# Kernel optimization log

Hardware: AMD Instinct MI355X
Metric: run time of the kernel (lower is better)

Reference implementation:

```python
import jax, jax.numpy as jnp
import numpy as np
from jax import lax

K = 7          # kernel_size
GROUPS = 16    # channels // group_channels
GC = 16        # group_channels
C = 256        # channels
PAD = (K - 1) // 2
BN_EPS = 1e-5


def setup_inputs() -> dict:
    key = jax.random.key(0)
    ks = jax.random.split(key, 8)
    B, H, W = 4, 56, 56
    x = jax.random.normal(ks[0], (B, C, H, W), jnp.float32)
    y = jax.random.normal(ks[1], (B, C, H, W), jnp.float32)
    # conv1: 1x1 conv (bias=False since followed by BN), C -> C//4
    w1 = jax.random.normal(ks[2], (C // 4, C), jnp.float32) * (1.0 / np.sqrt(C))
    gamma = jnp.ones((C // 4,), jnp.float32)
    beta = jnp.zeros((C // 4,), jnp.float32)
    mean = jax.random.normal(ks[3], (C // 4,), jnp.float32) * 0.1
    var = jax.random.uniform(ks[4], (C // 4,), jnp.float32, 0.5, 1.5)
    # conv2: 1x1 conv with bias, C//4 -> k^2 * groups
    w2 = jax.random.normal(ks[5], (K * K * GROUPS, C // 4), jnp.float32) * (1.0 / np.sqrt(C // 4))
    b2 = jnp.zeros((K * K * GROUPS,), jnp.float32)
    return {"x": x, "y": y, "w1": w1, "gamma": gamma, "beta": beta,
            "mean": mean, "var": var, "w2": w2, "b2": b2}


def reference(x, y, w1, gamma, beta, mean, var, w2, b2):
    # weight branch: 1x1 conv -> BN (inference) -> ReLU -> 1x1 conv
    t = jnp.einsum('oc,bchw->bohw', w1, x)                      # [B, C/4, H, W]
    scale = gamma * lax.rsqrt(var + BN_EPS)
    shift = beta - mean * scale
    t = jax.nn.relu(t * scale[None, :, None, None] + shift[None, :, None, None])
    weight = jnp.einsum('oc,bchw->bohw', w2, t) + b2[None, :, None, None]  # [B, k^2*G, H, W]
    B, _, H, W = weight.shape
    weight = weight.reshape(B, GROUPS, 1, K * K, H, W)

    # unfold y: patches channel order is (c, ki, kj) major-to-minor, matching torch unfold
    patches = lax.conv_general_dilated_patches(
        y, (K, K), (1, 1), [(PAD, PAD), (PAD, PAD)],
        dimension_numbers=('NCHW', 'OIHW', 'NCHW'))               # [B, C*k^2, H, W]
    patches = patches.reshape(B, GROUPS, GC, K * K, H, W)

    out = (weight * patches).sum(axis=3).reshape(B, C, H, W)
    return out
```

## Files before the change

### kernel.cpp

```cpp
#include <hip/hip_runtime.h>

#define HH 56
#define WW 56
#define HWSZ 3136
#define KS 7
#define KK 49

typedef __attribute__((ext_vector_type(8))) short short8;
typedef __attribute__((ext_vector_type(4))) float f32x4;

__device__ inline unsigned short f2bf(float f) {
    unsigned u = __builtin_bit_cast(unsigned, f);
    u += 0x7FFF + ((u >> 16) & 1);
    return (unsigned short)(u >> 16);
}
__device__ inline float bflo(unsigned u) { return __builtin_bit_cast(float, u << 16); }
__device__ inline float bfhi(unsigned u) { return __builtin_bit_cast(float, u & 0xFFFF0000u); }

#define XSTR 260
__global__ __launch_bounds__(256) void ka_mfma(
    const float* __restrict__ x, const float* __restrict__ w1,
    const float* __restrict__ gamma, const float* __restrict__ beta,
    const float* __restrict__ mean, const float* __restrict__ var,
    const float* __restrict__ w2,
    unsigned short* __restrict__ t_bf, unsigned short* __restrict__ w2p)
{
    const int tid = threadIdx.x;
    if (blockIdx.x >= 392) {
        const int g = blockIdx.x - 392;
        #pragma unroll
        for (int it = 0; it < 16; ++it) {
            const int i = it * 256 + tid;
            const int r = i >> 6, k = i & 63;
            float v = (r < KK) ? w2[(g * KK + r) * 64 + k] : 0.f;
            w2p[(size_t)(g * 64 + r) * 64 + k] = f2bf(v);
        }
        return;
    }

    __shared__ __align__(16) unsigned short xls[32 * XSTR];

    const int p0 = blockIdx.x * 32;
    const int b = p0 / HWSZ, hw0 = p0 - b * HWSZ;

    {
        const int pl = tid & 31, cb0 = tid >> 5;
        const float* xb = x + (size_t)b * 256 * HWSZ + hw0 + pl;
        #pragma unroll
        for (int ps = 0; ps < 4; ++ps) {
            const int cb = ps * 8 + cb0;
            const int c0 = cb * 8;
            unsigned u[4];
            #pragma unroll
            for (int j = 0; j < 4; ++j) {
                float va = xb[(size_t)(c0 + 2 * j) * HWSZ];
                float vb = xb[(size_t)(c0 + 2 * j + 1) * HWSZ];
                u[j] = (unsigned)f2bf(va) | ((unsigned)f2bf(vb) << 16);
            }
            *(uint4*)&xls[cb * XSTR + pl * 8] = make_uint4(u[0], u[1], u[2], u[3]);
        }
    }

    const int lane = tid & 63, wv = tid >> 6;
    const int m = lane & 15, q = lane >> 4;

    short8 af[8];
    {
        const float* wrow = w1 + (wv * 16 + m) * 256 + q * 8;
        #pragma unroll
        for (int ks = 0; ks < 8; ++ks) {
            float4 f0 = *(const float4*)(wrow + ks * 32);
            float4 f1 = *(const float4*)(wrow + ks * 32 + 4);
            short8 s;
            s[0] = (short)f2bf(f0.x); s[1] = (short)f2bf(f0.y);
            s[2] = (short)f2bf(f0.z); s[3] = (short)f2bf(f0.w);
            s[4] = (short)f2bf(f1.x); s[5] = (short)f2bf(f1.y);
            s[6] = (short)f2bf(f1.z); s[7] = (short)f2bf(f1.w);
            af[ks] = s;
        }
    }
    __syncthreads();

    #pragma unroll
    for (int nt = 0; nt < 2; ++nt) {
        f32x4 acc = {0.f, 0.f, 0.f, 0.f};
        #pragma unroll
        for (int ks = 0; ks < 8; ++ks) {
            short8 bfr = *(const short8*)&xls[(ks * 4 + q) * XSTR + (nt * 16 + m) * 8];
            acc = __builtin_amdgcn_mfma_f32_16x16x32_bf16(af[ks], bfr, acc, 0, 0, 0);
        }
        const int ob = wv * 16 + q * 4;
        float4 g4 = *(const float4*)&gamma[ob];
        float4 v4 = *(const float4*)&var[ob];
        float4 m4 = *(const float4*)&mean[ob];
        float4 b4 = *(const float4*)&beta[ob];
        float gg[4] = {g4.x, g4.y, g4.z, g4.w};
        float vv[4] = {v4.x, v4.y, v4.z, v4.w};
        float mm[4] = {m4.x, m4.y, m4.z, m4.w};
        float bb[4] = {b4.x, b4.y, b4.z, b4.w};
        unsigned r0 = 0, r1 = 0;
        #pragma unroll
        for (int j = 0; j < 4; ++j) {
            float sc = gg[j] * rsqrtf(vv[j] + 1e-5f);
            float sh = bb[j] - mm[j] * sc;
            float val = acc[j] * sc + sh;
            val = val > 0.f ? val : 0.f;
            unsigned hb = f2bf(val);
            if (j < 2) r0 |= hb << (16 * j);
            else       r1 |= hb << (16 * (j - 2));
        }
        const int p = p0 + nt * 16 + m;
        *(uint2*)&t_bf[(size_t)p * 64 + ob] = make_uint2(r0, r1);
    }
}

__global__ __launch_bounds__(256) void kb_fused(
    const float* __restrict__ y, const float* __restrict__ b2,
    const unsigned short* __restrict__ t_bf, const unsigned short* __restrict__ w2p,
    float* __restrict__ out)
{
    __shared__ __align__(16) unsigned short wgt[2 * 52 * 68];

    const int tid = threadIdx.x;
    const int gp = blockIdx.x & 7;
    const int bh = blockIdx.x >> 3;
    const int b = bh / HH, h = bh - b * HH;

    {
        const int lane = tid & 63, wv = tid >> 6;
        const int m = lane & 15, q = lane >> 4;
        #pragma unroll
        for (int it = 0; it < 2; ++it) {
            const int tsk = wv + 4 * it;
            const int gl = tsk >> 2, pt = tsk & 3;
            const int g = gp * 2 + gl;
            const int prow = b * HWSZ + h * WW + pt * 16 + m;
            const short8* ta = (const short8*)(t_bf + (size_t)prow * 64 + q * 8);
            short8 a0 = ta[0];
            short8 a1 = ta[4];
            f32x4 acc[4];
            #pragma unroll
            for (int mt = 0; mt < 4; ++mt) { acc[mt][0]=0.f; acc[mt][1]=0.f; acc[mt][2]=0.f; acc[mt][3]=0.f; }
            #pragma unroll
            for (int mt = 0; mt < 4; ++mt) {
                const short8* tb = (const short8*)(w2p +
                    (size_t)(g * 64 + mt * 16 + m) * 64 + q * 8);
                short8 b0 = tb[0], b1 = tb[4];
                acc[mt] = __builtin_amdgcn_mfma_f32_16x16x32_bf16(a0, b0, acc[mt], 0, 0, 0);
                acc[mt] = __builtin_amdgcn_mfma_f32_16x16x32_bf16(a1, b1, acc[mt], 0, 0, 0);
            }
            #pragma unroll
            for (int mt = 0; mt < 4; ++mt) {
                const int kk = mt * 16 + m;
                if (kk < 52) {
                    float bv = (kk < KK) ? b2[g * KK + kk] : 0.f;
                    f32x4 v = acc[mt];
                    unsigned r0 = (unsigned)f2bf(v[0] + bv) | ((unsigned)f2bf(v[1] + bv) << 16);
                    unsigned r1 = (unsigned)f2bf(v[2] + bv) | ((unsigned)f2bf(v[3] + bv) << 16);
                    const int pxb = pt * 16 + q * 4;
                    *(uint2*)&wgt[(gl * 52 + kk) * 68 + pxb] = make_uint2(r0, r1);
                }
            }
        }
    }
    __syncthreads();

    if (tid < 224) {
        const int gl = tid / 112;
        const int rem = tid - gl * 112;
        const int c2 = rem / 14, pq = rem - c2 * 14;
        const int g = gp * 2 + gl;
        const int cc0 = c2 * 2;
        const unsigned short* wg = &wgt[gl * 52 * 68 + pq * 4];
        const bool eL = (pq > 0), eR = (pq < 13);
        const int offL = eL ? 0 : 4;
        const int offR = eR ? 8 : 4;
        const float* yb0 = y + (size_t)(b * 256 + g * 16 + cc0) * HWSZ + pq * 4 - 4;
        const float* yb1 = yb0 + HWSZ;

        float4 cA0, cA1, cA2, cB0, cB1, cB2;
        float4 nA0, nA1, nA2, nB0, nB1, nB2;
        {
            const int hs = h - 3;
            const int hsc = hs < 0 ? 0 : hs;
            const float* r0 = yb0 + hsc * WW;
            const float* r1 = yb1 + hsc * WW;
            cA0 = *(const float4*)(r0 + offL);
            cA1 = *(const float4*)(r0 + 4);
            cA2 = *(const float4*)(r0 + offR);
            cB0 = *(const float4*)(r1 + offL);
            cB1 = *(const float4*)(r1 + 4);
            cB2 = *(const float4*)(r1 + offR);
        }
        float a00=0.f,a01=0.f,a02=0.f,a03=0.f;
        float a10=0.f,a11=0.f,a12=0.f,a13=0.f;

        #pragma unroll
        for (int di = 0; di < KS; ++di) {
            if (di < 6) {
                const int hs = h - 2 + di;
                const int hsc = hs < 0 ? 0 : (hs > HH - 1 ? HH - 1 : hs);
                const float* r0 = yb0 + hsc * WW;
                const float* r1 = yb1 + hsc * WW;
                nA0 = *(const float4*)(r0 + offL);
                nA1 = *(const float4*)(r0 + 4);
                nA2 = *(const float4*)(r0 + offR);
                nB0 = *(const float4*)(r1 + offL);
                nB1 = *(const float4*)(r1 + 4);
                nB2 = *(const float4*)(r1 + offR);
            }
            const int hs = h - 3 + di;
            if ((unsigned)hs < HH) {
                float w0[11], w1v[11];
                w0[1] = eL ? cA0.y : 0.f;  w0[2] = eL ? cA0.z : 0.f;  w0[3] = eL ? cA0.w : 0.f;
                w0[4] = cA1.x; w0[5] = cA1.y; w0[6] = cA1.z; w0[7] = cA1.w;
                w0[8] = eR ? cA2.x : 0.f;  w0[9] = eR ? cA2.y : 0.f;  w0[10] = eR ? cA2.z : 0.f;
                w1v[1] = eL ? cB0.y : 0.f; w1v[2] = eL ? cB0.z : 0.f; w1v[3] = eL ? cB0.w : 0.f;
                w1v[4] = cB1.x; w1v[5] = cB1.y; w1v[6] = cB1.z; w1v[7] = cB1.w;
                w1v[8] = eR ? cB2.x : 0.f; w1v[9] = eR ? cB2.y : 0.f; w1v[10] = eR ? cB2.z : 0.f;
                #pragma unroll
                for (int dj = 0; dj < KS; ++dj) {
                    uint2 wr = *(const uint2*)&wg[(di * KS + dj) * 68];
                    float g0 = bflo(wr.x), g1 = bfhi(wr.x);
                    float g2 = bflo(wr.y), g3 = bfhi(wr.y);
                    a00 += g0 * w0[dj + 1];  a01 += g1 * w0[dj + 2];
                    a02 += g2 * w0[dj + 3];  a03 += g3 * w0[dj + 4];
                    a10 += g0 * w1v[dj + 1]; a11 += g1 * w1v[dj + 2];
                    a12 += g2 * w1v[dj + 3]; a13 += g3 * w1v[dj + 4];
                }
            }
            if (di < 6) {
                cA0 = nA0; cA1 = nA1; cA2 = nA2;
                cB0 = nB0; cB1 = nB1; cB2 = nB2;
            }
        }
        float* o0 = out + (size_t)(b * 256 + g * 16 + cc0) * HWSZ + h * WW + pq * 4;
        *(float4*)o0 = make_float4(a00, a01, a02, a03);
        *(float4*)(o0 + HWSZ) = make_float4(a10, a11, a12, a13);
    }
}

extern "C" void kernel_launch(void* const* d_in, const int* in_sizes, int n_in,
                              void* d_out, int out_size, void* d_ws, size_t ws_size,
                              hipStream_t stream) {
    const float* x     = (const float*)d_in[0];
    const float* y     = (const float*)d_in[1];
    const float* w1    = (const float*)d_in[2];
    const float* gamma = (const float*)d_in[3];
    const float* beta  = (const float*)d_in[4];
    const float* mean  = (const float*)d_in[5];
    const float* var   = (const float*)d_in[6];
    const float* w2    = (const float*)d_in[7];
    const float* b2    = (const float*)d_in[8];
    float* out = (float*)d_out;

    unsigned short* t_bf = (unsigned short*)d_ws;
    unsigned short* w2p  = t_bf + (size_t)12608 * 64;

    ka_mfma<<<408, 256, 0, stream>>>(x, w1, gamma, beta, mean, var, w2, t_bf, w2p);
    kb_fused<<<1792, 256, 0, stream>>>(y, b2, t_bf, w2p, out);
}
```

Baseline: 43.09 us.

## Shrink per-block work in both kernels to double grid parallelism

```diff
diff --git a/kernel.cpp b/kernel.cpp
--- a/kernel.cpp
+++ b/kernel.cpp
@@ -17,7 +17,6 @@
 __device__ inline float bflo(unsigned u) { return __builtin_bit_cast(float, u << 16); }
 __device__ inline float bfhi(unsigned u) { return __builtin_bit_cast(float, u & 0xFFFF0000u); }
 
-#define XSTR 260
 __global__ __launch_bounds__(256) void ka_mfma(
     const float* __restrict__ x, const float* __restrict__ w1,
     const float* __restrict__ gamma, const float* __restrict__ beta,
@@ -26,8 +25,8 @@
     unsigned short* __restrict__ t_bf, unsigned short* __restrict__ w2p)
 {
     const int tid = threadIdx.x;
-    if (blockIdx.x >= 392) {
-        const int g = blockIdx.x - 392;
+    if (blockIdx.x < 16) {
+        const int g = blockIdx.x;
         #pragma unroll
         for (int it = 0; it < 16; ++it) {
             const int i = it * 256 + tid;
@@ -38,80 +37,60 @@
         return;
     }
 
-    __shared__ __align__(16) unsigned short xls[32 * XSTR];
-
-    const int p0 = blockIdx.x * 32;
+    const int tile = blockIdx.x - 16;
+    const int p0 = tile * 16;
     const int b = p0 / HWSZ, hw0 = p0 - b * HWSZ;
-
-    {
-        const int pl = tid & 31, cb0 = tid >> 5;
-        const float* xb = x + (size_t)b * 256 * HWSZ + hw0 + pl;
-        #pragma unroll
-        for (int ps = 0; ps < 4; ++ps) {
-            const int cb = ps * 8 + cb0;
-            const int c0 = cb * 8;
-            unsigned u[4];
-            #pragma unroll
-            for (int j = 0; j < 4; ++j) {
-                float va = xb[(size_t)(c0 + 2 * j) * HWSZ];
-                float vb = xb[(size_t)(c0 + 2 * j + 1) * HWSZ];
-                u[j] = (unsigned)f2bf(va) | ((unsigned)f2bf(vb) << 16);
-            }
-            *(uint4*)&xls[cb * XSTR + pl * 8] = make_uint4(u[0], u[1], u[2], u[3]);
-        }
-    }
 
     const int lane = tid & 63, wv = tid >> 6;
     const int m = lane & 15, q = lane >> 4;
 
-    short8 af[8];
-    {
-        const float* wrow = w1 + (wv * 16 + m) * 256 + q * 8;
-        #pragma unroll
-        for (int ks = 0; ks < 8; ++ks) {
-            float4 f0 = *(const float4*)(wrow + ks * 32);
-            float4 f1 = *(const float4*)(wrow + ks * 32 + 4);
-            short8 s;
-            s[0] = (short)f2bf(f0.x); s[1] = (short)f2bf(f0.y);
-            s[2] = (short)f2bf(f0.z); s[3] = (short)f2bf(f0.w);
-            s[4] = (short)f2bf(f1.x); s[5] = (short)f2bf(f1.y);
-            s[6] = (short)f2bf(f1.z); s[7] = (short)f2bf(f1.w);
-            af[ks] = s;
-        }
-    }
-    __syncthreads();
-
+    const float* xb   = x + (size_t)b * 256 * HWSZ + hw0 + m;
+    const float* wrow = w1 + (wv * 16 + m) * 256 + q * 8;
+
+    f32x4 acc = {0.f, 0.f, 0.f, 0.f};
     #pragma unroll
-    for (int nt = 0; nt < 2; ++nt) {
-        f32x4 acc = {0.f, 0.f, 0.f, 0.f};
-        #pragma unroll
-        for (int ks = 0; ks < 8; ++ks) {
-            short8 bfr = *(const short8*)&xls[(ks * 4 + q) * XSTR + (nt * 16 + m) * 8];
-            acc = __builtin_amdgcn_mfma_f32_16x16x32_bf16(af[ks], bfr, acc, 0, 0, 0);
-        }
-        const int ob = wv * 16 + q * 4;
-        float4 g4 = *(const float4*)&gamma[ob];
-        float4 v4 = *(const float4*)&var[ob];
-        float4 m4 = *(const float4*)&mean[ob];
-        float4 b4 = *(const float4*)&beta[ob];
-        float gg[4] = {g4.x, g4.y, g4.z, g4.w};
-        float vv[4] = {v4.x, v4.y, v4.z, v4.w};
-        float mm[4] = {m4.x, m4.y, m4.z, m4.w};
-        float bb[4] = {b4.x, b4.y, b4.z, b4.w};
-        unsigned r0 = 0, r1 = 0;
-        #pragma unroll
-        for (int j = 0; j < 4; ++j) {
-            float sc = gg[j] * rsqrtf(vv[j] + 1e-5f);
-            float sh = bb[j] - mm[j] * sc;
-            float val = acc[j] * sc + sh;
-            val = val > 0.f ? val : 0.f;
-            unsigned hb = f2bf(val);
-            if (j < 2) r0 |= hb << (16 * j);
-            else       r1 |= hb << (16 * (j - 2));
-        }
-        const int p = p0 + nt * 16 + m;
-        *(uint2*)&t_bf[(size_t)p * 64 + ob] = make_uint2(r0, r1);
-    }
+    for (int ks = 0; ks < 8; ++ks) {
+        const int c0 = ks * 32 + q * 8;
+        float xv[8];
+        #pragma unroll
+        for (int j = 0; j < 8; ++j)
+            xv[j] = xb[(size_t)(c0 + j) * HWSZ];
+        short8 bfr;
+        #pragma unroll
+        for (int j = 0; j < 8; ++j)
+            bfr[j] = (short)f2bf(xv[j]);
+        float4 f0 = *(const float4*)(wrow + ks * 32);
+        float4 f1 = *(const float4*)(wrow + ks * 32 + 4);
+        short8 afr;
+        afr[0] = (short)f2bf(f0.x); afr[1] = (short)f2bf(f0.y);
+        afr[2] = (short)f2bf(f0.z); afr[3] = (short)f2bf(f0.w);
+        afr[4] = (short)f2bf(f1.x); afr[5] = (short)f2bf(f1.y);
+        afr[6] = (short)f2bf(f1.z); afr[7] = (short)f2bf(f1.w);
+        acc = __builtin_amdgcn_mfma_f32_16x16x32_bf16(afr, bfr, acc, 0, 0, 0);
+    }
+
+    const int ob = wv * 16 + q * 4;
+    float4 g4 = *(const float4*)&gamma[ob];
+    float4 v4 = *(const float4*)&var[ob];
+    float4 m4 = *(const float4*)&mean[ob];
+    float4 b4 = *(const float4*)&beta[ob];
+    float gg[4] = {g4.x, g4.y, g4.z, g4.w};
+    float vv[4] = {v4.x, v4.y, v4.z, v4.w};
+    float mm[4] = {m4.x, m4.y, m4.z, m4.w};
+    float bb[4] = {b4.x, b4.y, b4.z, b4.w};
+    unsigned r0 = 0, r1 = 0;
+    #pragma unroll
+    for (int j = 0; j < 4; ++j) {
+        float sc = gg[j] * rsqrtf(vv[j] + 1e-5f);
+        float sh = bb[j] - mm[j] * sc;
+        float val = acc[j] * sc + sh;
+        val = val > 0.f ? val : 0.f;
+        unsigned hb = f2bf(val);
+        if (j < 2) r0 |= hb << (16 * j);
+        else       r1 |= hb << (16 * (j - 2));
+    }
+    const int p = p0 + m;
+    *(uint2*)&t_bf[(size_t)p * 64 + ob] = make_uint2(r0, r1);
 }
 
 __global__ __launch_bounds__(256) void kb_fused(
@@ -119,81 +98,65 @@
     const unsigned short* __restrict__ t_bf, const unsigned short* __restrict__ w2p,
     float* __restrict__ out)
 {
-    __shared__ __align__(16) unsigned short wgt[2 * 52 * 68];
+    __shared__ __align__(16) unsigned short wgt[52 * 68];
 
     const int tid = threadIdx.x;
-    const int gp = blockIdx.x & 7;
-    const int bh = blockIdx.x >> 3;
+    const int g = blockIdx.x & 15;
+    const int bh = blockIdx.x >> 4;
     const int b = bh / HH, h = bh - b * HH;
 
     {
         const int lane = tid & 63, wv = tid >> 6;
         const int m = lane & 15, q = lane >> 4;
-        #pragma unroll
-        for (int it = 0; it < 2; ++it) {
-            const int tsk = wv + 4 * it;
-            const int gl = tsk >> 2, pt = tsk & 3;
-            const int g = gp * 2 + gl;
-            const int prow = b * HWSZ + h * WW + pt * 16 + m;
-            const short8* ta = (const short8*)(t_bf + (size_t)prow * 64 + q * 8);
-            short8 a0 = ta[0];
-            short8 a1 = ta[4];
-            f32x4 acc[4];
-            #pragma unroll
-            for (int mt = 0; mt < 4; ++mt) { acc[mt][0]=0.f; acc[mt][1]=0.f; acc[mt][2]=0.f; acc[mt][3]=0.f; }
-            #pragma unroll
-            for (int mt = 0; mt < 4; ++mt) {
-                const short8* tb = (const short8*)(w2p +
-                    (size_t)(g * 64 + mt * 16 + m) * 64 + q * 8);
-                short8 b0 = tb[0], b1 = tb[4];
-                acc[mt] = __builtin_amdgcn_mfma_f32_16x16x32_bf16(a0, b0, acc[mt], 0, 0, 0);
-                acc[mt] = __builtin_amdgcn_mfma_f32_16x16x32_bf16(a1, b1, acc[mt], 0, 0, 0);
+        const int pt = wv;
+        const int prow = b * HWSZ + h * WW + pt * 16 + m;
+        const short8* ta = (const short8*)(t_bf + (size_t)prow * 64 + q * 8);
+        short8 a0 = ta[0];
+        short8 a1 = ta[4];
+        f32x4 acc[4];
+        #pragma unroll
+        for (int mt = 0; mt < 4; ++mt) { acc[mt][0]=0.f; acc[mt][1]=0.f; acc[mt][2]=0.f; acc[mt][3]=0.f; }
+        #pragma unroll
+        for (int mt = 0; mt < 4; ++mt) {
+            const short8* tb = (const short8*)(w2p +
+                (size_t)(g * 64 + mt * 16 + m) * 64 + q * 8);
+            short8 b0 = tb[0], b1 = tb[4];
+            acc[mt] = __builtin_amdgcn_mfma_f32_16x16x32_bf16(a0, b0, acc[mt], 0, 0, 0);
+            acc[mt] = __builtin_amdgcn_mfma_f32_16x16x32_bf16(a1, b1, acc[mt], 0, 0, 0);
+        }
+        #pragma unroll
+        for (int mt = 0; mt < 4; ++mt) {
+            const int kk = mt * 16 + m;
+            if (kk < 52) {
+                float bv = (kk < KK) ? b2[g * KK + kk] : 0.f;
+                f32x4 v = acc[mt];
+                unsigned r0 = (unsigned)f2bf(v[0] + bv) | ((unsigned)f2bf(v[1] + bv) << 16);
+                unsigned r1 = (unsigned)f2bf(v[2] + bv) | ((unsigned)f2bf(v[3] + bv) << 16);
+                const int pxb = pt * 16 + q * 4;
+                *(uint2*)&wgt[kk * 68 + pxb] = make_uint2(r0, r1);
             }
-            #pragma unroll
-            for (int mt = 0; mt < 4; ++mt) {
-                const int kk = mt * 16 + m;
-                if (kk < 52) {
-                    float bv = (kk < KK) ? b2[g * KK + kk] : 0.f;
-                    f32x4 v = acc[mt];
-                    unsigned r0 = (unsigned)f2bf(v[0] + bv) | ((unsigned)f2bf(v[1] + bv) << 16);
-                    unsigned r1 = (unsigned)f2bf(v[2] + bv) | ((unsigned)f2bf(v[3] + bv) << 16);
-                    const int pxb = pt * 16 + q * 4;
-                    *(uint2*)&wgt[(gl * 52 + kk) * 68 + pxb] = make_uint2(r0, r1);
-                }
-            }
         }
     }
     __syncthreads();
 
     if (tid < 224) {
-        const int gl = tid / 112;
-        const int rem = tid - gl * 112;
-        const int c2 = rem / 14, pq = rem - c2 * 14;
-        const int g = gp * 2 + gl;
-        const int cc0 = c2 * 2;
-        const unsigned short* wg = &wgt[gl * 52 * 68 + pq * 4];
+        const int cc = tid / 14, pq = tid - cc * 14;
+        const unsigned short* wg = &wgt[pq * 4];
         const bool eL = (pq > 0), eR = (pq < 13);
         const int offL = eL ? 0 : 4;
         const int offR = eR ? 8 : 4;
-        const float* yb0 = y + (size_t)(b * 256 + g * 16 + cc0) * HWSZ + pq * 4 - 4;
-        const float* yb1 = yb0 + HWSZ;
-
-        float4 cA0, cA1, cA2, cB0, cB1, cB2;
-        float4 nA0, nA1, nA2, nB0, nB1, nB2;
+        const float* yb0 = y + (size_t)(b * 256 + g * 16 + cc) * HWSZ + pq * 4 - 4;
+
+        float4 cA0, cA1, cA2, nA0, nA1, nA2;
         {
             const int hs = h - 3;
             const int hsc = hs < 0 ? 0 : hs;
             const float* r0 = yb0 + hsc * WW;
-            const float* r1 = yb1 + hsc * WW;
             cA0 = *(const float4*)(r0 + offL);
             cA1 = *(const float4*)(r0 + 4);
             cA2 = *(const float4*)(r0 + offR);
-            cB0 = *(const float4*)(r1 + offL);
-            cB1 = *(const float4*)(r1 + 4);
-            cB2 = *(const float4*)(r1 + offR);
-        }
-        float a00=0.f,a01=0.f,a02=0.f,a03=0.f;
-        float a10=0.f,a11=0.f,a12=0.f,a13=0.f;
+        }
+        float a00 = 0.f, a01 = 0.f, a02 = 0.f, a03 = 0.f;
 
         #pragma unroll
         for (int di = 0; di < KS; ++di) {
@@ -201,42 +164,29 @@
                 const int hs = h - 2 + di;
                 const int hsc = hs < 0 ? 0 : (hs > HH - 1 ? HH - 1 : hs);
                 const float* r0 = yb0 + hsc * WW;
-                const float* r1 = yb1 + hsc * WW;
                 nA0 = *(const float4*)(r0 + offL);
                 nA1 = *(const float4*)(r0 + 4);
                 nA2 = *(const float4*)(r0 + offR);
-                nB0 = *(const float4*)(r1 + offL);
-                nB1 = *(const float4*)(r1 + 4);
-                nB2 = *(const float4*)(r1 + offR);
             }
             const int hs = h - 3 + di;
             if ((unsigned)hs < HH) {
-                float w0[11], w1v[11];
+                float w0[11];
                 w0[1] = eL ? cA0.y : 0.f;  w0[2] = eL ? cA0.z : 0.f;  w0[3] = eL ? cA0.w : 0.f;
                 w0[4] = cA1.x; w0[5] = cA1.y; w0[6] = cA1.z; w0[7] = cA1.w;
                 w0[8] = eR ? cA2.x : 0.f;  w0[9] = eR ? cA2.y : 0.f;  w0[10] = eR ? cA2.z : 0.f;
-                w1v[1] = eL ? cB0.y : 0.f; w1v[2] = eL ? cB0.z : 0.f; w1v[3] = eL ? cB0.w : 0.f;
-                w1v[4] = cB1.x; w1v[5] = cB1.y; w1v[6] = cB1.z; w1v[7] = cB1.w;
-                w1v[8] = eR ? cB2.x : 0.f; w1v[9] = eR ? cB2.y : 0.f; w1v[10] = eR ? cB2.z : 0.f;
                 #pragma unroll
                 for (int dj = 0; dj < KS; ++dj) {
                     uint2 wr = *(const uint2*)&wg[(di * KS + dj) * 68];
-                    float g0 = bflo(wr.x), g1 = bfhi(wr.x);
-                    float g2 = bflo(wr.y), g3 = bfhi(wr.y);
-                    a00 += g0 * w0[dj + 1];  a01 += g1 * w0[dj + 2];
-                    a02 += g2 * w0[dj + 3];  a03 += g3 * w0[dj + 4];
-                    a10 += g0 * w1v[dj + 1]; a11 += g1 * w1v[dj + 2];
-                    a12 += g2 * w1v[dj + 3]; a13 += g3 * w1v[dj + 4];
+                    a00 += bflo(wr.x) * w0[dj + 1];
+                    a01 += bfhi(wr.x) * w0[dj + 2];
+                    a02 += bflo(wr.y) * w0[dj + 3];
+                    a03 += bfhi(wr.y) * w0[dj + 4];
                 }
             }
-            if (di < 6) {
-                cA0 = nA0; cA1 = nA1; cA2 = nA2;
-                cB0 = nB0; cB1 = nB1; cB2 = nB2;
-            }
-        }
-        float* o0 = out + (size_t)(b * 256 + g * 16 + cc0) * HWSZ + h * WW + pq * 4;
+            if (di < 6) { cA0 = nA0; cA1 = nA1; cA2 = nA2; }
+        }
+        float* o0 = out + (size_t)(b * 256 + g * 16 + cc) * HWSZ + h * WW + pq * 4;
         *(float4*)o0 = make_float4(a00, a01, a02, a03);
-        *(float4*)(o0 + HWSZ) = make_float4(a10, a11, a12, a13);
     }
 }
 
@@ -257,6 +207,6 @@
     unsigned short* t_bf = (unsigned short*)d_ws;
     unsigned short* w2p  = t_bf + (size_t)12608 * 64;
 
-    ka_mfma<<<408, 256, 0, stream>>>(x, w1, gamma, beta, mean, var, w2, t_bf, w2p);
-    kb_fused<<<1792, 256, 0, stream>>>(y, b2, t_bf, w2p, out);
-}
+    ka_mfma<<<800, 256, 0, stream>>>(x, w1, gamma, beta, mean, var, w2, t_bf, w2p);
+    kb_fused<<<3584, 256, 0, stream>>>(y, b2, t_bf, w2p, out);
+}
```

Result: slower. 46.32 us (+7.5%).
